# Performance work log

Measured on AMD Instinct MI355X. Metric: run time of the kernel, lower is better.

## Reference

```python
import jax, jax.numpy as jnp
import numpy as np

N_NODES = 100000
N_EDGES = 1600000
NEG_SLOPE = 0.2  # PyG GATConv default
BN_EPS = 1e-5


def gat_conv(x, src, dst, W, a_src, a_dst, bias):
    # x: [N, F], W: [F, H, C]
    h = jnp.einsum('nf,fhc->nhc', x, W)                 # [N, H, C]
    al_src = jnp.sum(h * a_src, axis=-1)                # [N, H]
    al_dst = jnp.sum(h * a_dst, axis=-1)                # [N, H]
    e = al_src[src] + al_dst[dst]                       # [E, H]
    e = jnp.where(e >= 0, e, NEG_SLOPE * e)             # leaky_relu(0.2)
    # segment softmax over incoming edges of each dst node
    emax = jax.ops.segment_max(e, dst, num_segments=N_NODES)
    ee = jnp.exp(e - emax[dst])
    denom = jax.ops.segment_sum(ee, dst, num_segments=N_NODES)
    alpha = ee / denom[dst]                             # [E, H]
    msg = alpha[:, :, None] * h[src]                    # [E, H, C]
    out = jax.ops.segment_sum(msg, dst, num_segments=N_NODES)  # [N, H, C]
    return out.mean(axis=1) + bias                      # concat=False -> head mean


def batch_norm(x, gamma, beta):
    mu = jnp.mean(x, axis=0)
    var = jnp.var(x, axis=0)  # biased, as in torch BN normalization
    return (x - mu) * jax.lax.rsqrt(var + BN_EPS) * gamma + beta


def setup_inputs() -> dict:
    key = jax.random.key(0)
    ks = jax.random.split(key, 16)
    inp = {
        'x': jax.random.normal(ks[0], (N_NODES, 128), jnp.float32),
        'edge_index': jax.random.randint(ks[1], (2, N_EDGES), 0, N_NODES, jnp.int64)
            if jax.config.jax_enable_x64 else
            jax.random.randint(ks[1], (2, N_EDGES), 0, N_NODES, jnp.int32),
        'edge_attr': jax.random.normal(ks[2], (N_EDGES, 8), jnp.float32),
        'W0': 0.1 * jax.random.normal(ks[3], (128, 4, 32), jnp.float32),
        'a_src0': 0.1 * jax.random.normal(ks[4], (4, 32), jnp.float32),
        'a_dst0': 0.1 * jax.random.normal(ks[5], (4, 32), jnp.float32),
        'b0': jnp.zeros((32,), jnp.float32),
        'g0': jnp.ones((32,), jnp.float32),
        'be0': jnp.zeros((32,), jnp.float32),
        'W1': 0.1 * jax.random.normal(ks[6], (32, 4, 32), jnp.float32),
        'a_src1': 0.1 * jax.random.normal(ks[7], (4, 32), jnp.float32),
        'a_dst1': 0.1 * jax.random.normal(ks[8], (4, 32), jnp.float32),
        'b1': jnp.zeros((32,), jnp.float32),
        'g1': jnp.ones((32,), jnp.float32),
        'be1': jnp.zeros((32,), jnp.float32),
        'W2': 0.1 * jax.random.normal(ks[9], (32, 4, 32), jnp.float32),
        'a_src2': 0.1 * jax.random.normal(ks[10], (4, 32), jnp.float32),
        'a_dst2': 0.1 * jax.random.normal(ks[11], (4, 32), jnp.float32),
        'b2': jnp.zeros((32,), jnp.float32),
    }
    return inp


def reference(x, edge_index, edge_attr, W0, a_src0, a_dst0, b0, g0, be0,
              W1, a_src1, a_dst1, b1, g1, be1, W2, a_src2, a_dst2, b2):
    src, dst = edge_index[0], edge_index[1]
    h = gat_conv(x, src, dst, W0, a_src0, a_dst0, b0)
    h = jax.nn.relu(batch_norm(h, g0, be0))  # dropout = identity (deterministic ref)
    h = gat_conv(h, src, dst, W1, a_src1, a_dst1, b1)
    h = jax.nn.relu(batch_norm(h, g1, be1))
    h = gat_conv(h, src, dst, W2, a_src2, a_dst2, b2)
    return (h, edge_attr)
```

## Files before the change

### kernel.cpp

```cpp
#include <hip/hip_runtime.h>
#include <cstdio>
#include <cstdint>

#define LRELU 0.2f
#define BN_EPS 1e-5f

typedef short bf16x8 __attribute__((ext_vector_type(8)));
typedef float f32x4 __attribute__((ext_vector_type(4)));

__device__ inline unsigned short f2bf(float f) {
  unsigned int u = __float_as_uint(f);
  u += 0x7fffu + ((u >> 16) & 1u);
  return (unsigned short)(u >> 16);
}
__device__ inline float bf2f(unsigned short v) {
  return __uint_as_float(((unsigned int)v) << 16);
}
__device__ inline float bflo(unsigned int u) { return __uint_as_float(u << 16); }
__device__ inline float bfhi(unsigned int u) { return __uint_as_float(u & 0xffff0000u); }


__global__ __launch_bounds__(256) void k_bhist_cast(
    const int* __restrict__ dst, int* __restrict__ bh, int E,
    const float* __restrict__ W0, const float* __restrict__ W1,
    const float* __restrict__ W2,
    unsigned short* __restrict__ Wt0, unsigned short* __restrict__ Wt1,
    unsigned short* __restrict__ Wt2) {
  __shared__ int cnt[512];
  const int gid = blockIdx.x * blockDim.x + threadIdx.x;
  if (gid < 24576) {
    int o = gid;
    if (o < 16384) {
      int n = o >> 7, k = o & 127;
      Wt0[o] = f2bf(W0[k * 128 + n]);
    } else if (o < 20480) {
      int p = o - 16384, n = p >> 5, k = p & 31;
      Wt1[p] = f2bf(W1[k * 128 + n]);
    } else {
      int p = o - 20480, n = p >> 5, k = p & 31;
      Wt2[p] = f2bf(W2[k * 128 + n]);
    }
  }
  for (int b = threadIdx.x; b < 512; b += 256) cnt[b] = 0;
  __syncthreads();
  const int gstride = gridDim.x * blockDim.x;
  for (int i = gid; i < E; i += gstride) atomicAdd(&cnt[dst[i] >> 8], 1);
  __syncthreads();
  for (int b = threadIdx.x; b < 512; b += 256)
    if (cnt[b]) atomicAdd(&bh[b], cnt[b]);
}

__device__ inline void scan_bh(const int* __restrict__ bh, int* pre, int* bsc) {
  const int t = threadIdx.x;
  const int a0 = bh[2 * t];
  const int a1 = bh[2 * t + 1];
  int s = a0 + a1;
  pre[t] = s;
  __syncthreads();
  for (int st = 1; st < 256; st <<= 1) {
    int u = (t >= st) ? pre[t - st] : 0;
    __syncthreads();
    pre[t] += u;
    __syncthreads();
  }
  const int ex = pre[t] - s;
  bsc[2 * t] = ex;
  bsc[2 * t + 1] = ex + a0;
  if (t == 255) bsc[512] = pre[255];
  __syncthreads();
}

__global__ __launch_bounds__(256) void k_bscatter(const int* __restrict__ src,
                                                  const int* __restrict__ dst,
                                                  const int* __restrict__ bh,
                                                  int* __restrict__ bclaim,
                                                  unsigned int* __restrict__ bpair,
                                                  int E) {
  __shared__ int pre[256];
  __shared__ int bsc[513];
  __shared__ int cnt[512];
  scan_bh(bh, pre, bsc);
  const int chunk = (E + gridDim.x - 1) / gridDim.x;
  const int beg = blockIdx.x * chunk;
  const int end = min(E, beg + chunk);
  for (int b = threadIdx.x; b < 512; b += 256) cnt[b] = 0;
  __syncthreads();
  for (int e = beg + threadIdx.x; e < end; e += 256)
    atomicAdd(&cnt[dst[e] >> 8], 1);
  __syncthreads();
  for (int b = threadIdx.x; b < 512; b += 256) {
    int c = cnt[b];
    cnt[b] = (c > 0) ? (bsc[b] + atomicAdd(&bclaim[b], c)) : 0;
  }
  __syncthreads();
  for (int e = beg + threadIdx.x; e < end; e += 256) {
    int d = dst[e];
    int pos = atomicAdd(&cnt[d >> 8], 1);
    bpair[pos] = ((unsigned)src[e] << 8) | ((unsigned)d & 255u);
  }
}

__global__ __launch_bounds__(256) void k_bcsr(const unsigned int* __restrict__ bpair,
                                              const int* __restrict__ bh,
                                              int* __restrict__ offs,
                                              int* __restrict__ srcs, int N, int E) {
  __shared__ int pre[256];
  __shared__ int bsc[513];
  __shared__ int sc[256];
  __shared__ int cur[256];
  scan_bh(bh, pre, bsc);
  const int b = blockIdx.x;
  const int lo = b << 8;
  const int t = threadIdx.x;
  const int e0 = bsc[b], e1 = bsc[b + 1];
  sc[t] = 0;
  __syncthreads();
  for (int e = e0 + t; e < e1; e += 256) atomicAdd(&sc[bpair[e] & 255u], 1);
  __syncthreads();
  int v = sc[t];
  for (int s = 1; s < 256; s <<= 1) {
    int u = (t >= s) ? sc[t - s] : 0;
    __syncthreads();
    sc[t] += u;
    __syncthreads();
  }
  const int pos0 = e0 + sc[t] - v;
  cur[t] = pos0;
  if (lo + t < N) offs[lo + t] = pos0;
  if (b == 0 && t == 0) offs[N] = E;
  __syncthreads();
  for (int e = e0 + t; e < e1; e += 256) {
    unsigned int p = bpair[e];
    int pos = atomicAdd(&cur[p & 255u], 1);
    srcs[pos] = (int)(p >> 8);
  }
}

template <int K, bool BN>
__global__ __launch_bounds__(256) void k_mfma(
    const float* __restrict__ Ain, const unsigned short* __restrict__ Wt,
    const float* __restrict__ asrc, const float* __restrict__ adst,
    const float* __restrict__ stats, const float* __restrict__ g,
    const float* __restrict__ be,
    unsigned short* __restrict__ h, float* __restrict__ als,
    float* __restrict__ ald, int N) {
  __shared__ unsigned short lsh[4][16 * 132];
  __shared__ float sc_s[32], sh_s[32];
  const int wv   = threadIdx.x >> 6;
  const int lane = threadIdx.x & 63;
  const int quad = lane >> 4;
  const int col  = lane & 15;
  const int m0   = blockIdx.x * 64 + wv * 16;
  const int rowc = min(m0 + col, N - 1);

  if constexpr (BN) {
    if (threadIdx.x < 32) {
      float s = 0.f, ss = 0.f;
#pragma unroll
      for (int r = 0; r < 8; r++) {
        s  += stats[r * 64 + threadIdx.x];
        ss += stats[r * 64 + 32 + threadIdx.x];
      }
      const float inv = 1.f / (float)N;
      const float mu = s * inv;
      const float var = ss * inv - mu * mu;
      const float scv = g[threadIdx.x] * rsqrtf(var + BN_EPS);
      sc_s[threadIdx.x] = scv;
      sh_s[threadIdx.x] = be[threadIdx.x] - mu * scv;
    }
    __syncthreads();
  }

  f32x4 acc[8];
#pragma unroll
  for (int t = 0; t < 8; t++) acc[t] = (f32x4){0.f, 0.f, 0.f, 0.f};

#pragma unroll
  for (int ks = 0; ks < K / 32; ks++) {
    const int k0 = ks * 32 + quad * 8;
    const float* ap = Ain + (size_t)rowc * K + k0;
    float4 f0 = *(const float4*)ap;
    float4 f1 = *(const float4*)(ap + 4);
    bf16x8 a;
    if constexpr (BN) {
      f0.x = fmaxf(0.f, fmaf(f0.x, sc_s[k0 + 0], sh_s[k0 + 0]));
      f0.y = fmaxf(0.f, fmaf(f0.y, sc_s[k0 + 1], sh_s[k0 + 1]));
      f0.z = fmaxf(0.f, fmaf(f0.z, sc_s[k0 + 2], sh_s[k0 + 2]));
      f0.w = fmaxf(0.f, fmaf(f0.w, sc_s[k0 + 3], sh_s[k0 + 3]));
      f1.x = fmaxf(0.f, fmaf(f1.x, sc_s[k0 + 4], sh_s[k0 + 4]));
      f1.y = fmaxf(0.f, fmaf(f1.y, sc_s[k0 + 5], sh_s[k0 + 5]));
      f1.z = fmaxf(0.f, fmaf(f1.z, sc_s[k0 + 6], sh_s[k0 + 6]));
      f1.w = fmaxf(0.f, fmaf(f1.w, sc_s[k0 + 7], sh_s[k0 + 7]));
    }
    a[0] = (short)f2bf(f0.x); a[1] = (short)f2bf(f0.y);
    a[2] = (short)f2bf(f0.z); a[3] = (short)f2bf(f0.w);
    a[4] = (short)f2bf(f1.x); a[5] = (short)f2bf(f1.y);
    a[6] = (short)f2bf(f1.z); a[7] = (short)f2bf(f1.w);
#pragma unroll
    for (int t = 0; t < 8; t++) {
      bf16x8 b = *(const bf16x8*)(Wt + (size_t)(t * 16 + col) * K + k0);
      acc[t] = __builtin_amdgcn_mfma_f32_16x16x32_bf16(a, b, acc[t], 0, 0, 0);
    }
  }

#pragma unroll
  for (int t = 0; t < 8; t++) {
#pragma unroll
    for (int j = 0; j < 4; j++)
      lsh[wv][(quad * 4 + j) * 132 + col + 16 * t] = f2bf(acc[t][j]);
  }
  __syncthreads();

  float as8[8], ad8[8];
#pragma unroll
  for (int j = 0; j < 8; j++) {
    as8[j] = asrc[col * 8 + j];
    ad8[j] = adst[col * 8 + j];
  }

#pragma unroll
  for (int i = 0; i < 4; i++) {
    const int row = i * 4 + quad;
    const int hrow = m0 + row;
    const unsigned short* rp = &lsh[wv][row * 132 + col * 8];
    ushort4 lo = *(const ushort4*)rp;
    ushort4 hi = *(const ushort4*)(rp + 4);
    float p = 0.f, q = 0.f, v;
    v = bf2f(lo.x); p += v * as8[0]; q += v * ad8[0];
    v = bf2f(lo.y); p += v * as8[1]; q += v * ad8[1];
    v = bf2f(lo.z); p += v * as8[2]; q += v * ad8[2];
    v = bf2f(lo.w); p += v * as8[3]; q += v * ad8[3];
    v = bf2f(hi.x); p += v * as8[4]; q += v * ad8[4];
    v = bf2f(hi.y); p += v * as8[5]; q += v * ad8[5];
    v = bf2f(hi.z); p += v * as8[6]; q += v * ad8[6];
    v = bf2f(hi.w); p += v * as8[7]; q += v * ad8[7];
    if (hrow < N) {
      ushort4* gp = (ushort4*)(h + (size_t)hrow * 128 + col * 8);
      gp[0] = lo; gp[1] = hi;
    }
    p += __shfl_xor(p, 1); p += __shfl_xor(p, 2);
    q += __shfl_xor(q, 1); q += __shfl_xor(q, 2);
    if ((lane & 3) == 0 && hrow < N) {
      const int head = col >> 2;
      als[hrow * 4 + head] = p;
      ald[hrow * 4 + head] = q;
    }
  }
}

template <bool STATS>
__global__ __launch_bounds__(256) void k_agg(
    const unsigned int* __restrict__ h2, const float* __restrict__ als,
    const float* __restrict__ ald, const int* __restrict__ offs,
    const int* __restrict__ srcs, const float* __restrict__ bias,
    float* __restrict__ y, float* __restrict__ stats, int N) {
  __shared__ float s1[32], s2[32];
  const int node = blockIdx.x * 4 + (threadIdx.x >> 6);
  const int lane = threadIdx.x & 63;
  const bool valid = node < N;
  if constexpr (STATS) {
    if (threadIdx.x < 32) { s1[threadIdx.x] = 0.f; s2[threadIdx.x] = 0.f; }
    __syncthreads();
  } else {
    if (!valid) return;
  }

  if (valid) {
    const int half = lane >> 5;
    const int sub  = lane & 31;
    const int head = sub >> 3;
    const int beg = __builtin_amdgcn_readfirstlane(offs[node]);
    const int end = __builtin_amdgcn_readfirstlane(offs[node + 1]);
    const float ad = ald[node * 4 + head];
    float ax0 = 0.f, ax1 = 0.f, ax2 = 0.f, ax3 = 0.f, dn = 0.f;

    for (int base = beg; base < end; base += 64) {
      const int mm = min(64, end - base);
      const int sv = srcs[base + min(lane, mm - 1)];
      const int vlim = mm - half;

      float aA0, aA1, aA2, aA3, aB0, aB1, aB2, aB3;
      uint2 uA0, uA1, uA2, uA3, uB0, uB1, uB2, uB3;
      int iA0, iA1, iA2, iA3, iB0, iB1, iB2, iB3;

#define SLOT(S, K, I)                                                      \
  {                                                                        \
    i##S##K = (I);                                                         \
    const int c0 = min((I), mm - 1), c1 = min((I) + 1, mm - 1);            \
    const int sA_ = __builtin_amdgcn_readlane(sv, c0);                     \
    const int sB_ = __builtin_amdgcn_readlane(sv, c1);                     \
    const int s_ = half ? sB_ : sA_;                                       \
    a##S##K = als[s_ * 4 + head];                                          \
    u##S##K = *(const uint2*)(h2 + (size_t)s_ * 64 + (sub << 1));          \
  }
#define ISSUE(S, J0) SLOT(S, 0, (J0)) SLOT(S, 1, (J0) + 2)                 \
                     SLOT(S, 2, (J0) + 4) SLOT(S, 3, (J0) + 6)
#define CSLOT(S, K)                                                        \
  {                                                                        \
    float e_ = a##S##K + ad;                                               \
    e_ = fmaxf(e_, LRELU * e_);                                            \
    float w_ = __expf(e_);                                                 \
    w_ = (i##S##K < vlim) ? w_ : 0.f;                                      \
    dn += w_;                                                              \
    ax0 = fmaf(w_, bflo(u##S##K.x), ax0);                                  \
    ax1 = fmaf(w_, bfhi(u##S##K.x), ax1);                                  \
    ax2 = fmaf(w_, bflo(u##S##K.y), ax2);                                  \
    ax3 = fmaf(w_, bfhi(u##S##K.y), ax3);                                  \
  }
#define COMPUTE(S) CSLOT(S, 0) CSLOT(S, 1) CSLOT(S, 2) CSLOT(S, 3)

      int j0 = 0;
      ISSUE(A, 0)
      j0 = 8;
      if (j0 >= mm) {
        COMPUTE(A)
      } else {
        for (;;) {
          ISSUE(B, j0) COMPUTE(A)
          j0 += 8;
          if (j0 >= mm) { COMPUTE(B) break; }
          ISSUE(A, j0) COMPUTE(B)
          j0 += 8;
          if (j0 >= mm) { COMPUTE(A) break; }
        }
      }
#undef SLOT
#undef ISSUE
#undef CSLOT
#undef COMPUTE
    }

    dn += __shfl_xor(dn, 32);
    const float r = (dn > 0.f) ? (1.f / dn) : 0.f;
    ax0 *= r; ax1 *= r; ax2 *= r; ax3 *= r;
    ax0 += __shfl_xor(ax0, 32); ax1 += __shfl_xor(ax1, 32);
    ax2 += __shfl_xor(ax2, 32); ax3 += __shfl_xor(ax3, 32);
    ax0 += __shfl_xor(ax0, 8);  ax1 += __shfl_xor(ax1, 8);
    ax2 += __shfl_xor(ax2, 8);  ax3 += __shfl_xor(ax3, 8);
    ax0 += __shfl_xor(ax0, 16); ax1 += __shfl_xor(ax1, 16);
    ax2 += __shfl_xor(ax2, 16); ax3 += __shfl_xor(ax3, 16);

    if (lane < 8) {
      float4 b4 = ((const float4*)bias)[lane];
      float4 o;
      o.x = 0.25f * ax0 + b4.x;
      o.y = 0.25f * ax1 + b4.y;
      o.z = 0.25f * ax2 + b4.z;
      o.w = 0.25f * ax3 + b4.w;
      ((float4*)(y + (size_t)node * 32))[lane] = o;
      if constexpr (STATS) {
        atomicAdd(&s1[4 * lane + 0], o.x); atomicAdd(&s2[4 * lane + 0], o.x * o.x);
        atomicAdd(&s1[4 * lane + 1], o.y); atomicAdd(&s2[4 * lane + 1], o.y * o.y);
        atomicAdd(&s1[4 * lane + 2], o.z); atomicAdd(&s2[4 * lane + 2], o.z * o.z);
        atomicAdd(&s1[4 * lane + 3], o.w); atomicAdd(&s2[4 * lane + 3], o.w * o.w);
      }
    }
  }

  if constexpr (STATS) {
    __syncthreads();
    if (threadIdx.x < 32) {
      float* sb = stats + (blockIdx.x & 7) * 64;
      atomicAdd(&sb[threadIdx.x], s1[threadIdx.x]);
      atomicAdd(&sb[32 + threadIdx.x], s2[threadIdx.x]);
    }
  }
}

__global__ void k_copy4(const f32x4* __restrict__ s, f32x4* __restrict__ d, int n) {
  int i = blockIdx.x * blockDim.x + threadIdx.x;
  if (i < n) {
    f32x4 v = __builtin_nontemporal_load(&s[i]);
    __builtin_nontemporal_store(v, &d[i]);
  }
}

extern "C" void kernel_launch(void* const* d_in, const int* in_sizes, int n_in,
                              void* d_out, int out_size, void* d_ws, size_t ws_size,
                              hipStream_t stream) {
  const float* x   = (const float*)d_in[0];
  const int*   ei  = (const int*)d_in[1];
  const float* ea  = (const float*)d_in[2];
  const float* W0  = (const float*)d_in[3];
  const float* as0 = (const float*)d_in[4];
  const float* ad0 = (const float*)d_in[5];
  const float* b0  = (const float*)d_in[6];
  const float* g0  = (const float*)d_in[7];
  const float* be0 = (const float*)d_in[8];
  const float* W1  = (const float*)d_in[9];
  const float* as1 = (const float*)d_in[10];
  const float* ad1 = (const float*)d_in[11];
  const float* b1  = (const float*)d_in[12];
  const float* g1  = (const float*)d_in[13];
  const float* be1 = (const float*)d_in[14];
  const float* W2  = (const float*)d_in[15];
  const float* as2 = (const float*)d_in[16];
  const float* ad2 = (const float*)d_in[17];
  const float* b2  = (const float*)d_in[18];

  const int N = in_sizes[0] / 128;
  const int E = in_sizes[1] / 2;
  const int* srcI = ei;
  const int* dstI = ei + E;
  const int NB = (N + 255) >> 8;

  char* w = (char*)d_ws;
  auto carve = [&](size_t bytes) -> void* {
    void* p = (void*)w;
    w += (bytes + 255) & ~(size_t)255;
    return p;
  };
  unsigned short* h  = (unsigned short*)carve((size_t)N * 128 * 2);
  float* als        = (float*)carve((size_t)N * 4 * 4);
  float* ald        = (float*)carve((size_t)N * 4 * 4);
  float* y          = (float*)carve((size_t)N * 32 * 4);
  int* offs         = (int*)carve((size_t)(N + 1) * 4);
  int* srcs         = (int*)carve((size_t)E * 4);
  int* bh           = (int*)carve(512 * 4);
  int* bclaim       = (int*)carve(512 * 4);
  float* stats      = (float*)carve(1024 * 4);
  char* zend        = w;
  unsigned short* Wt0 = (unsigned short*)carve(128 * 128 * 2);
  unsigned short* Wt1 = (unsigned short*)carve(128 * 32 * 2);
  unsigned short* Wt2 = (unsigned short*)carve(128 * 32 * 2);
  if ((size_t)(w - (char*)d_ws) > ws_size) {
    fprintf(stderr, "GAT kernel: ws too small (%zu needed, %zu given)\n",
            (size_t)(w - (char*)d_ws), ws_size);
    return;
  }
  unsigned int* bpair = (unsigned int*)h;

  float* out_nodes = (float*)d_out;
  float* out_ea    = out_nodes + (size_t)N * 32;

  (void)hipMemsetAsync(bh, 0, (size_t)(zend - (char*)bh), stream);

  k_bhist_cast<<<512, 256, 0, stream>>>(dstI, bh, E, W0, W1, W2, Wt0, Wt1, Wt2);
  k_bscatter<<<384, 256, 0, stream>>>(srcI, dstI, bh, bclaim, bpair, E);
  k_bcsr<<<NB, 256, 0, stream>>>(bpair, bh, offs, srcs, N, E);

  const int gGemm = (N + 63) / 64;
  const int gAgg  = (N + 3) / 4;

  k_mfma<128, false><<<gGemm, 256, 0, stream>>>(x, Wt0, as0, ad0,
                                                nullptr, nullptr, nullptr,
                                                h, als, ald, N);
  k_agg<true><<<gAgg, 256, 0, stream>>>((const unsigned int*)h, als, ald, offs,
                                        srcs, b0, y, stats, N);
  k_mfma<32, true><<<gGemm, 256, 0, stream>>>(y, Wt1, as1, ad1, stats, g0, be0,
                                              h, als, ald, N);
  k_agg<true><<<gAgg, 256, 0, stream>>>((const unsigned int*)h, als, ald, offs,
                                        srcs, b1, y, stats + 512, N);
  k_mfma<32, true><<<gGemm, 256, 0, stream>>>(y, Wt2, as2, ad2, stats + 512, g1, be1,
                                              h, als, ald, N);
  k_agg<false><<<gAgg, 256, 0, stream>>>((const unsigned int*)h, als, ald, offs,
                                         srcs, b2, out_nodes, nullptr, N);
  const int n4 = E * 2;
  k_copy4<<<(n4 + 255) / 256, 256, 0, stream>>>((const f32x4*)ea, (f32x4*)out_ea, n4);
}
```

Before: 576.6 us.

## Fuse edge_attr copy into histogram kernel and split aggregation launches in halves

The separate edge_attr passthrough copy kernel is removed and its copy loop folded into the histogram/weight-cast kernel, which now launches with 2048 blocks. The bscatter grid grows from 384 to 512 blocks. Each aggregation launch is split into two launches over node halves on the same stream. This saves one launch and overlaps the streaming copy with the histogram atomics, but the extra agg launches add launch overhead with no obvious concurrency gain, since they are serialized on one stream.

Result: slower. 615.2 us (+6.7%).

```diff
diff --git a/kernel.cpp b/kernel.cpp
--- a/kernel.cpp
+++ b/kernel.cpp
@@ -20,14 +20,16 @@
 __device__ inline float bfhi(unsigned int u) { return __uint_as_float(u & 0xffff0000u); }
 
 
-__global__ __launch_bounds__(256) void k_bhist_cast(
+__global__ __launch_bounds__(256) void k_bhist_cast_copy(
     const int* __restrict__ dst, int* __restrict__ bh, int E,
     const float* __restrict__ W0, const float* __restrict__ W1,
     const float* __restrict__ W2,
     unsigned short* __restrict__ Wt0, unsigned short* __restrict__ Wt1,
-    unsigned short* __restrict__ Wt2) {
+    unsigned short* __restrict__ Wt2,
+    const f32x4* __restrict__ ea, f32x4* __restrict__ oea) {
   __shared__ int cnt[512];
   const int gid = blockIdx.x * blockDim.x + threadIdx.x;
+  const int gstride = gridDim.x * blockDim.x;
   if (gid < 24576) {
     int o = gid;
     if (o < 16384) {
@@ -43,8 +45,12 @@
   }
   for (int b = threadIdx.x; b < 512; b += 256) cnt[b] = 0;
   __syncthreads();
-  const int gstride = gridDim.x * blockDim.x;
   for (int i = gid; i < E; i += gstride) atomicAdd(&cnt[dst[i] >> 8], 1);
+  const int n4 = E * 2;
+  for (int i = gid; i < n4; i += gstride) {
+    f32x4 v = __builtin_nontemporal_load(&ea[i]);
+    __builtin_nontemporal_store(v, &oea[i]);
+  }
   __syncthreads();
   for (int b = threadIdx.x; b < 512; b += 256)
     if (cnt[b]) atomicAdd(&bh[b], cnt[b]);
@@ -253,11 +259,11 @@
     const unsigned int* __restrict__ h2, const float* __restrict__ als,
     const float* __restrict__ ald, const int* __restrict__ offs,
     const int* __restrict__ srcs, const float* __restrict__ bias,
-    float* __restrict__ y, float* __restrict__ stats, int N) {
+    float* __restrict__ y, float* __restrict__ stats, int node0, int nend) {
   __shared__ float s1[32], s2[32];
-  const int node = blockIdx.x * 4 + (threadIdx.x >> 6);
+  const int node = node0 + blockIdx.x * 4 + (threadIdx.x >> 6);
   const int lane = threadIdx.x & 63;
-  const bool valid = node < N;
+  const bool valid = node < nend;
   if constexpr (STATS) {
     if (threadIdx.x < 32) { s1[threadIdx.x] = 0.f; s2[threadIdx.x] = 0.f; }
     __syncthreads();
@@ -364,14 +370,6 @@
       atomicAdd(&sb[threadIdx.x], s1[threadIdx.x]);
       atomicAdd(&sb[32 + threadIdx.x], s2[threadIdx.x]);
     }
-  }
-}
-
-__global__ void k_copy4(const f32x4* __restrict__ s, f32x4* __restrict__ d, int n) {
-  int i = blockIdx.x * blockDim.x + threadIdx.x;
-  if (i < n) {
-    f32x4 v = __builtin_nontemporal_load(&s[i]);
-    __builtin_nontemporal_store(v, &d[i]);
   }
 }
 
@@ -435,26 +433,34 @@
 
   (void)hipMemsetAsync(bh, 0, (size_t)(zend - (char*)bh), stream);
 
-  k_bhist_cast<<<512, 256, 0, stream>>>(dstI, bh, E, W0, W1, W2, Wt0, Wt1, Wt2);
-  k_bscatter<<<384, 256, 0, stream>>>(srcI, dstI, bh, bclaim, bpair, E);
+  k_bhist_cast_copy<<<2048, 256, 0, stream>>>(dstI, bh, E, W0, W1, W2,
+                                              Wt0, Wt1, Wt2,
+                                              (const f32x4*)ea, (f32x4*)out_ea);
+  k_bscatter<<<512, 256, 0, stream>>>(srcI, dstI, bh, bclaim, bpair, E);
   k_bcsr<<<NB, 256, 0, stream>>>(bpair, bh, offs, srcs, N, E);
 
   const int gGemm = (N + 63) / 64;
-  const int gAgg  = (N + 3) / 4;
+  const int halfN = ((N / 2) + 3) & ~3;
+  const int gA0 = (halfN + 3) / 4;
+  const int gA1 = (N - halfN + 3) / 4;
 
   k_mfma<128, false><<<gGemm, 256, 0, stream>>>(x, Wt0, as0, ad0,
                                                 nullptr, nullptr, nullptr,
                                                 h, als, ald, N);
-  k_agg<true><<<gAgg, 256, 0, stream>>>((const unsigned int*)h, als, ald, offs,
-                                        srcs, b0, y, stats, N);
+  k_agg<true><<<gA0, 256, 0, stream>>>((const unsigned int*)h, als, ald, offs,
+                                       srcs, b0, y, stats, 0, halfN);
+  k_agg<true><<<gA1, 256, 0, stream>>>((const unsigned int*)h, als, ald, offs,
+                                       srcs, b0, y, stats, halfN, N);
   k_mfma<32, true><<<gGemm, 256, 0, stream>>>(y, Wt1, as1, ad1, stats, g0, be0,
                                               h, als, ald, N);
-  k_agg<true><<<gAgg, 256, 0, stream>>>((const unsigned int*)h, als, ald, offs,
-                                        srcs, b1, y, stats + 512, N);
+  k_agg<true><<<gA0, 256, 0, stream>>>((const unsigned int*)h, als, ald, offs,
+                                       srcs, b1, y, stats + 512, 0, halfN);
+  k_agg<true><<<gA1, 256, 0, stream>>>((const unsigned int*)h, als, ald, offs,
+                                       srcs, b1, y, stats + 512, halfN, N);
   k_mfma<32, true><<<gGemm, 256, 0, stream>>>(y, Wt2, as2, ad2, stats + 512, g1, be1,
                                               h, als, ald, N);
-  k_agg<false><<<gAgg, 256, 0, stream>>>((const unsigned int*)h, als, ald, offs,
-                                         srcs, b2, out_nodes, nullptr, N);
-  const int n4 = E * 2;
-  k_copy4<<<(n4 + 255) / 256, 256, 0, stream>>>((const f32x4*)ea, (f32x4*)out_ea, n4);
-}
+  k_agg<false><<<gA0, 256, 0, stream>>>((const unsigned int*)h, als, ald, offs,
+                                        srcs, b2, out_nodes, nullptr, 0, halfN);
+  k_agg<false><<<gA1, 256, 0, stream>>>((const unsigned int*)h, als, ald, offs,
+                                        srcs, b2, out_nodes, nullptr, halfN, N);
+}
```

## Fuse edge_attr copy into histogram kernel and double rows per GEMM block

Applied to the files above, without the earlier changes.

The standalone edge_attr passthrough copy is folded into the histogram/weight-cast kernel, which now launches with more blocks and grid-strides over the copy, removing one kernel launch. The MFMA GEMM kernel now processes two 64-row tiles per block, reusing each loaded weight fragment for two MFMAs and halving the grid size. The bscatter launch grid is also enlarged. This raises register pressure in the GEMM and adds copy traffic to the histogram kernel, whose atomics may now contend with the streaming copy.

Result: no change. 580.9 us (+0.7%).

```diff
diff --git a/kernel.cpp b/kernel.cpp
--- a/kernel.cpp
+++ b/kernel.cpp
@@ -20,14 +20,16 @@
 __device__ inline float bfhi(unsigned int u) { return __uint_as_float(u & 0xffff0000u); }
 
 
-__global__ __launch_bounds__(256) void k_bhist_cast(
+__global__ __launch_bounds__(256) void k_bhist_cast_copy(
     const int* __restrict__ dst, int* __restrict__ bh, int E,
     const float* __restrict__ W0, const float* __restrict__ W1,
     const float* __restrict__ W2,
     unsigned short* __restrict__ Wt0, unsigned short* __restrict__ Wt1,
-    unsigned short* __restrict__ Wt2) {
+    unsigned short* __restrict__ Wt2,
+    const f32x4* __restrict__ ea, f32x4* __restrict__ oea) {
   __shared__ int cnt[512];
   const int gid = blockIdx.x * blockDim.x + threadIdx.x;
+  const int gstride = gridDim.x * blockDim.x;
   if (gid < 24576) {
     int o = gid;
     if (o < 16384) {
@@ -43,8 +45,12 @@
   }
   for (int b = threadIdx.x; b < 512; b += 256) cnt[b] = 0;
   __syncthreads();
-  const int gstride = gridDim.x * blockDim.x;
   for (int i = gid; i < E; i += gstride) atomicAdd(&cnt[dst[i] >> 8], 1);
+  const int n4 = E * 2;
+  for (int i = gid; i < n4; i += gstride) {
+    f32x4 v = __builtin_nontemporal_load(&ea[i]);
+    __builtin_nontemporal_store(v, &oea[i]);
+  }
   __syncthreads();
   for (int b = threadIdx.x; b < 512; b += 256)
     if (cnt[b]) atomicAdd(&bh[b], cnt[b]);
@@ -150,8 +156,10 @@
   const int lane = threadIdx.x & 63;
   const int quad = lane >> 4;
   const int col  = lane & 15;
-  const int m0   = blockIdx.x * 64 + wv * 16;
-  const int rowc = min(m0 + col, N - 1);
+  const int m0   = blockIdx.x * 128 + wv * 16;
+  const int m1   = m0 + 64;
+  const int rowc0 = min(m0 + col, N - 1);
+  const int rowc1 = min(m1 + col, N - 1);
 
   if constexpr (BN) {
     if (threadIdx.x < 32) {
@@ -171,45 +179,56 @@
     __syncthreads();
   }
 
-  f32x4 acc[8];
+  f32x4 acc0[8], acc1[8];
 #pragma unroll
-  for (int t = 0; t < 8; t++) acc[t] = (f32x4){0.f, 0.f, 0.f, 0.f};
+  for (int t = 0; t < 8; t++) {
+    acc0[t] = (f32x4){0.f, 0.f, 0.f, 0.f};
+    acc1[t] = (f32x4){0.f, 0.f, 0.f, 0.f};
+  }
 
 #pragma unroll
   for (int ks = 0; ks < K / 32; ks++) {
     const int k0 = ks * 32 + quad * 8;
-    const float* ap = Ain + (size_t)rowc * K + k0;
-    float4 f0 = *(const float4*)ap;
-    float4 f1 = *(const float4*)(ap + 4);
-    bf16x8 a;
+    const float* ap0 = Ain + (size_t)rowc0 * K + k0;
+    const float* ap1 = Ain + (size_t)rowc1 * K + k0;
+    float4 f0 = *(const float4*)ap0;
+    float4 f1 = *(const float4*)(ap0 + 4);
+    float4 e0 = *(const float4*)ap1;
+    float4 e1 = *(const float4*)(ap1 + 4);
     if constexpr (BN) {
-      f0.x = fmaxf(0.f, fmaf(f0.x, sc_s[k0 + 0], sh_s[k0 + 0]));
-      f0.y = fmaxf(0.f, fmaf(f0.y, sc_s[k0 + 1], sh_s[k0 + 1]));
-      f0.z = fmaxf(0.f, fmaf(f0.z, sc_s[k0 + 2], sh_s[k0 + 2]));
-      f0.w = fmaxf(0.f, fmaf(f0.w, sc_s[k0 + 3], sh_s[k0 + 3]));
-      f1.x = fmaxf(0.f, fmaf(f1.x, sc_s[k0 + 4], sh_s[k0 + 4]));
-      f1.y = fmaxf(0.f, fmaf(f1.y, sc_s[k0 + 5], sh_s[k0 + 5]));
-      f1.z = fmaxf(0.f, fmaf(f1.z, sc_s[k0 + 6], sh_s[k0 + 6]));
-      f1.w = fmaxf(0.f, fmaf(f1.w, sc_s[k0 + 7], sh_s[k0 + 7]));
-    }
-    a[0] = (short)f2bf(f0.x); a[1] = (short)f2bf(f0.y);
-    a[2] = (short)f2bf(f0.z); a[3] = (short)f2bf(f0.w);
-    a[4] = (short)f2bf(f1.x); a[5] = (short)f2bf(f1.y);
-    a[6] = (short)f2bf(f1.z); a[7] = (short)f2bf(f1.w);
+      const float s0 = sc_s[k0 + 0], h0 = sh_s[k0 + 0];
+      const float s1 = sc_s[k0 + 1], h1 = sh_s[k0 + 1];
+      const float s2 = sc_s[k0 + 2], h2 = sh_s[k0 + 2];
+      const float s3 = sc_s[k0 + 3], h3 = sh_s[k0 + 3];
+      const float s4 = sc_s[k0 + 4], h4 = sh_s[k0 + 4];
+      const float s5 = sc_s[k0 + 5], h5 = sh_s[k0 + 5];
+      const float s6 = sc_s[k0 + 6], h6 = sh_s[k0 + 6];
+      const float s7 = sc_s[k0 + 7], h7 = sh_s[k0 + 7];
+      f0.x = fmaxf(0.f, fmaf(f0.x, s0, h0)); e0.x = fmaxf(0.f, fmaf(e0.x, s0, h0));
+      f0.y = fmaxf(0.f, fmaf(f0.y, s1, h1)); e0.y = fmaxf(0.f, fmaf(e0.y, s1, h1));
+      f0.z = fmaxf(0.f, fmaf(f0.z, s2, h2)); e0.z = fmaxf(0.f, fmaf(e0.z, s2, h2));
+      f0.w = fmaxf(0.f, fmaf(f0.w, s3, h3)); e0.w = fmaxf(0.f, fmaf(e0.w, s3, h3));
+      f1.x = fmaxf(0.f, fmaf(f1.x, s4, h4)); e1.x = fmaxf(0.f, fmaf(e1.x, s4, h4));
+      f1.y = fmaxf(0.f, fmaf(f1.y, s5, h5)); e1.y = fmaxf(0.f, fmaf(e1.y, s5, h5));
+      f1.z = fmaxf(0.f, fmaf(f1.z, s6, h6)); e1.z = fmaxf(0.f, fmaf(e1.z, s6, h6));
+      f1.w = fmaxf(0.f, fmaf(f1.w, s7, h7)); e1.w = fmaxf(0.f, fmaf(e1.w, s7, h7));
+    }
+    bf16x8 a0, a1;
+    a0[0] = (short)f2bf(f0.x); a0[1] = (short)f2bf(f0.y);
+    a0[2] = (short)f2bf(f0.z); a0[3] = (short)f2bf(f0.w);
+    a0[4] = (short)f2bf(f1.x); a0[5] = (short)f2bf(f1.y);
+    a0[6] = (short)f2bf(f1.z); a0[7] = (short)f2bf(f1.w);
+    a1[0] = (short)f2bf(e0.x); a1[1] = (short)f2bf(e0.y);
+    a1[2] = (short)f2bf(e0.z); a1[3] = (short)f2bf(e0.w);
+    a1[4] = (short)f2bf(e1.x); a1[5] = (short)f2bf(e1.y);
+    a1[6] = (short)f2bf(e1.z); a1[7] = (short)f2bf(e1.w);
 #pragma unroll
     for (int t = 0; t < 8; t++) {
       bf16x8 b = *(const bf16x8*)(Wt + (size_t)(t * 16 + col) * K + k0);
-      acc[t] = __builtin_amdgcn_mfma_f32_16x16x32_bf16(a, b, acc[t], 0, 0, 0);
-    }
-  }
-
-#pragma unroll
-  for (int t = 0; t < 8; t++) {
-#pragma unroll
-    for (int j = 0; j < 4; j++)
-      lsh[wv][(quad * 4 + j) * 132 + col + 16 * t] = f2bf(acc[t][j]);
-  }
-  __syncthreads();
+      acc0[t] = __builtin_amdgcn_mfma_f32_16x16x32_bf16(a0, b, acc0[t], 0, 0, 0);
+      acc1[t] = __builtin_amdgcn_mfma_f32_16x16x32_bf16(a1, b, acc1[t], 0, 0, 0);
+    }
+  }
 
   float as8[8], ad8[8];
 #pragma unroll
@@ -218,34 +237,44 @@
     ad8[j] = adst[col * 8 + j];
   }
 
-#pragma unroll
-  for (int i = 0; i < 4; i++) {
-    const int row = i * 4 + quad;
-    const int hrow = m0 + row;
-    const unsigned short* rp = &lsh[wv][row * 132 + col * 8];
-    ushort4 lo = *(const ushort4*)rp;
-    ushort4 hi = *(const ushort4*)(rp + 4);
-    float p = 0.f, q = 0.f, v;
-    v = bf2f(lo.x); p += v * as8[0]; q += v * ad8[0];
-    v = bf2f(lo.y); p += v * as8[1]; q += v * ad8[1];
-    v = bf2f(lo.z); p += v * as8[2]; q += v * ad8[2];
-    v = bf2f(lo.w); p += v * as8[3]; q += v * ad8[3];
-    v = bf2f(hi.x); p += v * as8[4]; q += v * ad8[4];
-    v = bf2f(hi.y); p += v * as8[5]; q += v * ad8[5];
-    v = bf2f(hi.z); p += v * as8[6]; q += v * ad8[6];
-    v = bf2f(hi.w); p += v * as8[7]; q += v * ad8[7];
-    if (hrow < N) {
-      ushort4* gp = (ushort4*)(h + (size_t)hrow * 128 + col * 8);
-      gp[0] = lo; gp[1] = hi;
-    }
-    p += __shfl_xor(p, 1); p += __shfl_xor(p, 2);
-    q += __shfl_xor(q, 1); q += __shfl_xor(q, 2);
-    if ((lane & 3) == 0 && hrow < N) {
-      const int head = col >> 2;
-      als[hrow * 4 + head] = p;
-      ald[hrow * 4 + head] = q;
-    }
-  }
+#define EPILOGUE(MM, ACC)                                                    \
+  {                                                                          \
+    _Pragma("unroll") for (int t = 0; t < 8; t++) {                          \
+      _Pragma("unroll") for (int j = 0; j < 4; j++)                          \
+          lsh[wv][(quad * 4 + j) * 132 + col + 16 * t] = f2bf(ACC[t][j]);    \
+    }                                                                        \
+    _Pragma("unroll") for (int i = 0; i < 4; i++) {                          \
+      const int row = i * 4 + quad;                                          \
+      const int hrow = (MM) + row;                                           \
+      const unsigned short* rp = &lsh[wv][row * 132 + col * 8];              \
+      ushort4 lo = *(const ushort4*)rp;                                      \
+      ushort4 hi = *(const ushort4*)(rp + 4);                                \
+      float p = 0.f, q = 0.f, v;                                             \
+      v = bf2f(lo.x); p += v * as8[0]; q += v * ad8[0];                      \
+      v = bf2f(lo.y); p += v * as8[1]; q += v * ad8[1];                      \
+      v = bf2f(lo.z); p += v * as8[2]; q += v * ad8[2];                      \
+      v = bf2f(lo.w); p += v * as8[3]; q += v * ad8[3];                      \
+      v = bf2f(hi.x); p += v * as8[4]; q += v * ad8[4];                      \
+      v = bf2f(hi.y); p += v * as8[5]; q += v * ad8[5];                      \
+      v = bf2f(hi.z); p += v * as8[6]; q += v * ad8[6];                      \
+      v = bf2f(hi.w); p += v * as8[7]; q += v * ad8[7];                      \
+      if (hrow < N) {                                                        \
+        ushort4* gp = (ushort4*)(h + (size_t)hrow * 128 + col * 8);          \
+        gp[0] = lo; gp[1] = hi;                                              \
+      }                                                                      \
+      p += __shfl_xor(p, 1); p += __shfl_xor(p, 2);                          \
+      q += __shfl_xor(q, 1); q += __shfl_xor(q, 2);                          \
+      if ((lane & 3) == 0 && hrow < N) {                                     \
+        const int head = col >> 2;                                           \
+        als[hrow * 4 + head] = p;                                            \
+        ald[hrow * 4 + head] = q;                                            \
+      }                                                                      \
+    }                                                                        \
+  }
+
+  EPILOGUE(m0, acc0)
+  EPILOGUE(m1, acc1)
+#undef EPILOGUE
 }
 
 template <bool STATS>
@@ -364,14 +393,6 @@
       atomicAdd(&sb[threadIdx.x], s1[threadIdx.x]);
       atomicAdd(&sb[32 + threadIdx.x], s2[threadIdx.x]);
     }
-  }
-}
-
-__global__ void k_copy4(const f32x4* __restrict__ s, f32x4* __restrict__ d, int n) {
-  int i = blockIdx.x * blockDim.x + threadIdx.x;
-  if (i < n) {
-    f32x4 v = __builtin_nontemporal_load(&s[i]);
-    __builtin_nontemporal_store(v, &d[i]);
   }
 }
 
@@ -435,11 +456,13 @@
 
   (void)hipMemsetAsync(bh, 0, (size_t)(zend - (char*)bh), stream);
 
-  k_bhist_cast<<<512, 256, 0, stream>>>(dstI, bh, E, W0, W1, W2, Wt0, Wt1, Wt2);
-  k_bscatter<<<384, 256, 0, stream>>>(srcI, dstI, bh, bclaim, bpair, E);
+  k_bhist_cast_copy<<<2048, 256, 0, stream>>>(dstI, bh, E, W0, W1, W2,
+                                              Wt0, Wt1, Wt2,
+                                              (const f32x4*)ea, (f32x4*)out_ea);
+  k_bscatter<<<512, 256, 0, stream>>>(srcI, dstI, bh, bclaim, bpair, E);
   k_bcsr<<<NB, 256, 0, stream>>>(bpair, bh, offs, srcs, N, E);
 
-  const int gGemm = (N + 63) / 64;
+  const int gGemm = (N + 127) / 128;
   const int gAgg  = (N + 3) / 4;
 
   k_mfma<128, false><<<gGemm, 256, 0, stream>>>(x, Wt0, as0, ad0,
@@ -455,6 +478,4 @@
                                               h, als, ald, N);
   k_agg<false><<<gAgg, 256, 0, stream>>>((const unsigned int*)h, als, ald, offs,
                                          srcs, b2, out_nodes, nullptr, N);
-  const int n4 = E * 2;
-  k_copy4<<<(n4 + 255) / 256, 256, 0, stream>>>((const f32x4*)ea, (f32x4*)out_ea, n4);
-}
+}
```
